# Performance work log

Hardware: AMD Instinct MI355X
Metric: run time of the kernel (lower is better)

Reference implementation:

```python
import jax, jax.numpy as jnp
import numpy as np

B, S, D = 2, 2048, 1024
H = 16
HD = D // H  # 64
THETA = 10000.0


def apply_rope(x, positions, theta):
    # x: (b, h, s, hd); positions: (s,)
    hd = x.shape[-1]
    inv_freq = theta ** (-jnp.arange(0, hd, 2, dtype=jnp.float32) / hd)  # (hd/2,)
    angles = positions.astype(jnp.float32)[:, None] * inv_freq[None, :]  # (s, hd/2)
    cos, sin = jnp.cos(angles), jnp.sin(angles)
    x1 = x[..., 0::2]
    x2 = x[..., 1::2]
    r1 = x1 * cos - x2 * sin
    r2 = x1 * sin + x2 * cos
    out = jnp.stack([r1, r2], axis=-1).reshape(x.shape)
    return out.astype(x.dtype)


def setup_inputs() -> dict:
    key = jax.random.key(0)
    ks = jax.random.split(key, 5)
    scale = 1.0 / np.sqrt(D)
    return {
        "in_features": jax.random.normal(ks[0], (B, S, D), dtype=jnp.float32),
        "token_positions": jnp.arange(S, dtype=jnp.int32),
        "Wq": jax.random.normal(ks[1], (D, D), dtype=jnp.float32) * scale,
        "Wk": jax.random.normal(ks[2], (D, D), dtype=jnp.float32) * scale,
        "Wv": jax.random.normal(ks[3], (D, D), dtype=jnp.float32) * scale,
        "Wo": jax.random.normal(ks[4], (D, D), dtype=jnp.float32) * scale,
    }


def reference(in_features, token_positions, Wq, Wk, Wv, Wo):
    b, s, d = in_features.shape
    h, hd = H, HD
    # bias-free linear: y = x @ W.T  (W is (out, in))
    q = in_features @ Wq.T
    k = in_features @ Wk.T
    v = in_features @ Wv.T
    # (b, s, h*hd) -> (b, h, s, hd)
    split = lambda t: t.reshape(b, s, h, hd).transpose(0, 2, 1, 3)
    q, k, v = split(q), split(k), split(v)
    q = apply_rope(q, token_positions, THETA)
    k = apply_rope(k, token_positions, THETA)
    scores = jnp.einsum("bhid,bhjd->bhij", q, k) / jnp.sqrt(jnp.asarray(hd, dtype=q.dtype))
    causal = jnp.triu(jnp.ones((s, s), dtype=bool), k=1)
    scores = jnp.where(causal, -jnp.inf, scores)
    attn = jax.nn.softmax(scores, axis=-1)
    out = jnp.einsum("bhij,bhjd->bhid", attn, v)
    out = out.transpose(0, 2, 1, 3).reshape(b, s, d)
    return out @ Wo.T
```

## Files before the change

### kernel.cpp

```cpp
#include <hip/hip_runtime.h>
#include <math.h>

#define NUM_HEADS 16
#define HEAD_DIM 64

typedef __bf16 bf16x8 __attribute__((ext_vector_type(8)));
typedef short shortx4 __attribute__((ext_vector_type(4)));
typedef float floatx4 __attribute__((ext_vector_type(4)));

#if __has_builtin(__builtin_amdgcn_exp2f)
#define EXP2(x) __builtin_amdgcn_exp2f(x)
#else
#define EXP2(x) exp2f(x)
#endif

__device__ __forceinline__ unsigned short f2b(float f) {
  unsigned int u = __float_as_uint(f);
  u += 0x7fffu + ((u >> 16) & 1u);
  return (unsigned short)(u >> 16);
}

__device__ __forceinline__ void async16(const void* g, void* l) {
  __builtin_amdgcn_global_load_lds(
      (const __attribute__((address_space(1))) unsigned int*)g,
      (__attribute__((address_space(3))) unsigned int*)l, 16, 0, 0);
}

__device__ __forceinline__ void cvt4(const float* in, unsigned short* out, int i) {
  float4 v = ((const float4*)in)[i];
  ushort4 o;
  o.x = f2b(v.x); o.y = f2b(v.y); o.z = f2b(v.z); o.w = f2b(v.w);
  ((ushort4*)out)[i] = o;
}

__global__ void prep(const float* __restrict__ x,
                     const float* __restrict__ w0, const float* __restrict__ w1,
                     const float* __restrict__ w2, const float* __restrict__ w3,
                     const int* __restrict__ pos,
                     unsigned short* Xb, unsigned short* o0, unsigned short* o1,
                     unsigned short* o2, unsigned short* o3,
                     float* __restrict__ tab, int xq, int w4, int ntab) {
  int i = blockIdx.x * 256 + threadIdx.x;
  int z = blockIdx.y;
  if (z == 0) {
    if (i < xq) {
#pragma unroll
      for (int rep = 0; rep < 4; ++rep) cvt4(x, Xb, rep * xq + i);
    }
  } else if (z <= 4) {
    if (i < w4) {
      const float* in = (z == 1) ? w0 : (z == 2) ? w1 : (z == 3) ? w2 : w3;
      unsigned short* out = (z == 1) ? o0 : (z == 2) ? o1 : (z == 3) ? o2 : o3;
      cvt4(in, out, i);
    }
  } else {
    if (i < ntab) {
      int fi = i & 31, s = i >> 5;
      float inv = expf(-0.28782313662425575f * (float)fi);
      float ang = (float)pos[s] * inv;
      float sn, cs;
      sincosf(ang, &sn, &cs);
      tab[i * 2] = cs;
      tab[i * 2 + 1] = sn;
    }
  }
}

template <int MODE, int MT>
__global__ __launch_bounds__(256, MODE == 1 ? 4 : 2)
void gemm_bt(const unsigned short* __restrict__ A,
             const unsigned short* __restrict__ B0,
             const unsigned short* __restrict__ B1,
             const unsigned short* __restrict__ B2,
             void* out0v, void* out1v, void* out2v,
             const float* __restrict__ ctab,
             int M, int N, int K, int S) {
  constexpr int ABUF = (MT / 16) * 512;
  constexpr int BBUF = 8 * 512;
  __shared__ unsigned short As[3 * ABUF];
  __shared__ unsigned short Bs[3 * BBUF];
  const int tid = threadIdx.x;
  const int lane = tid & 63;
  const int w = tid >> 6;
  const int lane16 = lane & 15;
  const int g = lane >> 4;
  const int wm = w >> 1, wn = w & 1;
  const int m0 = blockIdx.y * MT;
  const int n0 = blockIdx.x * 128;
  const unsigned short* Bp = (blockIdx.z == 0) ? B0 : (blockIdx.z == 1 ? B1 : B2);
  constexpr int MTILES = MT / 32;

  const floatx4 vzero = {0.f, 0.f, 0.f, 0.f};
  floatx4 acc[MTILES][4];
#pragma unroll
  for (int i = 0; i < MTILES; i++)
#pragma unroll
    for (int j = 0; j < 4; j++) acc[i][j] = vzero;

  const int ar = lane >> 2;
  const int ac = (lane & 3) * 8;

  auto stageg = [&](int k0, int sbi) {
    if constexpr (MT == 128) {
#pragma unroll
      for (int c = 0; c < 2; c++) {
        int chunk = w * 2 + c;
        async16(A  + (size_t)(m0 + chunk * 16 + ar) * K + k0 + ac, As + sbi * ABUF + chunk * 512);
        async16(Bp + (size_t)(n0 + chunk * 16 + ar) * K + k0 + ac, Bs + sbi * BBUF + chunk * 512);
      }
    } else {
      async16(A  + (size_t)(m0 + w * 16 + ar) * K + k0 + ac, As + sbi * ABUF + w * 512);
      async16(Bp + (size_t)(n0 + w * 16 + ar) * K + k0 + ac, Bs + sbi * BBUF + w * 512);
      async16(Bp + (size_t)(n0 + (w + 4) * 16 + ar) * K + k0 + ac, Bs + sbi * BBUF + (w + 4) * 512);
    }
  };

  const int NK = K >> 5;
  stageg(0, 0);
  __builtin_amdgcn_sched_barrier(0);
  if (NK > 1) stageg(32, 1);
  __builtin_amdgcn_sched_barrier(0);

  int bi = 0, si = 2;
  for (int ks = 0; ks < NK; ++ks) {
    if (ks < NK - 1) {
      if constexpr (MT == 128) asm volatile("s_waitcnt vmcnt(4)" ::: "memory");
      else                     asm volatile("s_waitcnt vmcnt(3)" ::: "memory");
    } else {
      asm volatile("s_waitcnt vmcnt(0)" ::: "memory");
    }
    __builtin_amdgcn_sched_barrier(0);
    __builtin_amdgcn_s_barrier();
    __builtin_amdgcn_sched_barrier(0);
    if (ks + 2 < NK) stageg((ks + 2) << 5, si);
    __builtin_amdgcn_sched_barrier(0);

    const unsigned short* Ab = As + bi * ABUF;
    const unsigned short* Bb = Bs + bi * BBUF;
    bf16x8 a[MTILES], b[4];
#pragma unroll
    for (int mt = 0; mt < MTILES; mt++)
      a[mt] = *(const bf16x8*)&Ab[(wm * (MT / 2) + mt * 16 + lane16) * 32 + g * 8];
#pragma unroll
    for (int nt = 0; nt < 4; nt++)
      b[nt] = *(const bf16x8*)&Bb[(wn * 64 + nt * 16 + lane16) * 32 + g * 8];
#pragma unroll
    for (int mt = 0; mt < MTILES; mt++)
#pragma unroll
      for (int nt = 0; nt < 4; nt++)
        acc[mt][nt] = __builtin_amdgcn_mfma_f32_16x16x32_bf16(b[nt], a[mt], acc[mt][nt], 0, 0, 0);

    bi = (bi == 2) ? 0 : bi + 1;
    si = (si == 2) ? 0 : si + 1;
  }

  if (MODE == 0) {
    if (blockIdx.z < 2) {
      unsigned short* outp = (unsigned short*)((blockIdx.z == 0) ? out0v : out1v);
      const float qs = (blockIdx.z == 0) ? 0.18033688011112042f : 1.0f;
#pragma unroll
      for (int mt = 0; mt < MTILES; mt++) {
        int m = m0 + wm * (MT / 2) + mt * 16 + lane16;
        int bb = m / S, s = m - bb * S;
        const float* crow = ctab + (size_t)s * 64;
#pragma unroll
        for (int nt = 0; nt < 4; nt++) {
          int n = n0 + wn * 64 + nt * 16 + g * 4;
          int h = n >> 6, dl = n & 63;
          floatx4 v = acc[mt][nt];
          float4 cs = *(const float4*)&crow[dl];
          float r0 = (v[0] * cs.x - v[1] * cs.y) * qs;
          float r1 = (v[0] * cs.y + v[1] * cs.x) * qs;
          float r2 = (v[2] * cs.z - v[3] * cs.w) * qs;
          float r3 = (v[2] * cs.w + v[3] * cs.z) * qs;
          shortx4 st;
          st[0] = (short)f2b(r0); st[1] = (short)f2b(r1);
          st[2] = (short)f2b(r2); st[3] = (short)f2b(r3);
          *(shortx4*)&outp[(((size_t)(bb * NUM_HEADS + h) * S + s) << 6) + dl] = st;
        }
      }
    } else {
      unsigned short* outp = (unsigned short*)out2v;
#pragma unroll
      for (int mt = 0; mt < MTILES; mt++) {
        int m = m0 + wm * (MT / 2) + mt * 16 + lane16;
        int bb = m / S, s = m - bb * S;
#pragma unroll
        for (int nt = 0; nt < 4; nt++) {
          int n = n0 + wn * 64 + nt * 16 + g * 4;
          int bh = bb * NUM_HEADS + (n >> 6);
          int dl = n & 63;
          size_t dbase = ((size_t)bh * 64 + dl) * S + s;
#pragma unroll
          for (int r = 0; r < 4; r++)
            outp[dbase + (size_t)r * S] = f2b(acc[mt][nt][r]);
        }
      }
    }
  } else {
    float* outp = (float*)out0v;
#pragma unroll
    for (int mt = 0; mt < MTILES; mt++) {
      int m = m0 + wm * (MT / 2) + mt * 16 + lane16;
#pragma unroll
      for (int nt = 0; nt < 4; nt++) {
        int n = n0 + wn * 64 + nt * 16 + g * 4;
        *(floatx4*)&outp[(size_t)m * N + n] = acc[mt][nt];
      }
    }
  }
}

__global__ __launch_bounds__(256, 2)
void flash_attn7(const unsigned short* __restrict__ Q,
                 const unsigned short* __restrict__ Kv,
                 const unsigned short* __restrict__ Vt,
                 unsigned short* __restrict__ Oattn, int S) {
  __shared__ unsigned short Ks[4 * 4096];
  __shared__ unsigned short Vs[4 * 4096];
  const int tid = threadIdx.x;
  const int lane = tid & 63;
  const int w = tid >> 6;
  const int lane16 = lane & 15;
  const int g = lane >> 4;
  const int sw = lane16 & 7;
  const int NT = S >> 6;
  int qa, bh;
  {
    int nx = gridDim.x, ny = gridDim.y;
    int flat = blockIdx.y * nx + blockIdx.x;
    if ((ny & 7) == 0) {
      int xcd = flat & 7;
      int idx = flat >> 3;
      int per = ny >> 3;
      bh = xcd * per + (idx % per);
      qa = idx / per;
    } else {
      qa = blockIdx.x; bh = blockIdx.y;
    }
  }
  const int qb = NT - 1 - qa;
  const int b = bh >> 4, h = bh & 15;
  const size_t kbase = (size_t)bh * S * HEAD_DIM;
  const unsigned short* Kbase = Kv + kbase;
  const unsigned short* Vtbase = Vt + (size_t)bh * HEAD_DIM * S;
  const int qrowA = qa * 64 + w * 16;
  const int qrowB = qb * 64 + w * 16;

  bf16x8 qA0, qA1, qB0, qB1;
  {
    const unsigned short* qp = Q + kbase + (size_t)(qrowA + lane16) * HEAD_DIM + g * 8;
    qA0 = *(const bf16x8*)qp;
    qA1 = *(const bf16x8*)(qp + 32);
    qp = Q + kbase + (size_t)(qrowB + lane16) * HEAD_DIM + g * 8;
    qB0 = *(const bf16x8*)qp;
    qB1 = *(const bf16x8*)(qp + 32);
  }

  const int ci0 = w * 64 + lane;
  const int ci1 = ci0 + 256;
  const int r0 = ci0 >> 3, j0 = (ci0 & 7) ^ (r0 & 7);
  const int r1 = ci1 >> 3, j1 = (ci1 & 7) ^ (r1 & 7);
  const unsigned short* kS0 = Kbase + r0 * HEAD_DIM + j0 * 8;
  const unsigned short* kS1 = Kbase + r1 * HEAD_DIM + j1 * 8;
  const unsigned short* vS0 = Vtbase + (size_t)r0 * S + j0 * 8;
  const unsigned short* vS1 = Vtbase + (size_t)r1 * S + j1 * 8;
  unsigned short* kD0 = Ks + ci0 * 8;
  unsigned short* kD1 = Ks + ci1 * 8;
  unsigned short* vD0 = Vs + ci0 * 8;
  unsigned short* vD1 = Vs + ci1 * 8;

  auto stage = [&](int t, int bi) {
    int koff = t * 4096;
    int voff = t * 64;
    int doff = bi * 4096;
    async16(kS0 + koff, kD0 + doff);
    async16(kS1 + koff, kD1 + doff);
    async16(vS0 + voff, vD0 + doff);
    async16(vS1 + voff, vD1 + doff);
  };

  const floatx4 vzero = {0.f, 0.f, 0.f, 0.f};
  floatx4 oA[4], oB[4];
#pragma unroll
  for (int i = 0; i < 4; i++) { oA[i] = vzero; oB[i] = vzero; }
  float lA = 0.f, lB = 0.f;

  stage(0, 0);
  __builtin_amdgcn_sched_barrier(0);
  if (qb >= 1) stage(1, 1);
  __builtin_amdgcn_sched_barrier(0);
  if (qb >= 2) stage(2, 2);
  __builtin_amdgcn_sched_barrier(0);

  for (int t = 0; t <= qb; ++t) {
    const int bi = t & 3;
    const int rem = qb - t;
    if (rem >= 2)      asm volatile("s_waitcnt vmcnt(8)" ::: "memory");
    else if (rem == 1) asm volatile("s_waitcnt vmcnt(4)" ::: "memory");
    else               asm volatile("s_waitcnt vmcnt(0)" ::: "memory");
    __builtin_amdgcn_sched_barrier(0);
    __builtin_amdgcn_s_barrier();
    __builtin_amdgcn_sched_barrier(0);
    if (t + 3 <= qb) stage(t + 3, (t + 3) & 3);
    __builtin_amdgcn_sched_barrier(0);

    const unsigned short* Kb_ = Ks + bi * 4096;
    const unsigned short* Vb_ = Vs + bi * 4096;
    const bool doA = (t <= qa);

    bf16x8 kf0[4], kf1[4];
#pragma unroll
    for (int c = 0; c < 4; ++c) {
      int rr = c * 16 + lane16;
      kf0[c] = *(const bf16x8*)&Kb_[(rr * 8 + (g ^ sw)) * 8];
      kf1[c] = *(const bf16x8*)&Kb_[(rr * 8 + ((4 + g) ^ sw)) * 8];
    }

    floatx4 scB[4];
#pragma unroll
    for (int c = 0; c < 4; ++c) {
      floatx4 s = vzero;
      s = __builtin_amdgcn_mfma_f32_16x16x32_bf16(kf0[c], qB0, s, 0, 0, 0);
      s = __builtin_amdgcn_mfma_f32_16x16x32_bf16(kf1[c], qB1, s, 0, 0, 0);
      scB[c] = s;
    }
    if (t == qb) {
      const int i = qrowB + lane16;
      const int jb = t * 64;
#pragma unroll
      for (int c = 0; c < 4; ++c)
#pragma unroll
        for (int r = 0; r < 4; ++r)
          if (jb + c * 16 + g * 4 + r > i) scB[c][r] = -INFINITY;
    }
    shortx4 pcB[4], pcA[4];
#pragma unroll
    for (int c = 0; c < 4; ++c) {
      float p0 = EXP2(scB[c][0]);
      float p1 = EXP2(scB[c][1]);
      float p2 = EXP2(scB[c][2]);
      float p3 = EXP2(scB[c][3]);
      lB += (p0 + p1) + (p2 + p3);
      union { unsigned int u[2]; shortx4 s4; } pu;
      pu.u[0] = __builtin_amdgcn_perm(__float_as_uint(p1), __float_as_uint(p0), 0x07060302u);
      pu.u[1] = __builtin_amdgcn_perm(__float_as_uint(p3), __float_as_uint(p2), 0x07060302u);
      pcB[c] = pu.s4;
    }

    if (doA) {
      floatx4 scA[4];
#pragma unroll
      for (int c = 0; c < 4; ++c) {
        floatx4 s = vzero;
        s = __builtin_amdgcn_mfma_f32_16x16x32_bf16(kf0[c], qA0, s, 0, 0, 0);
        s = __builtin_amdgcn_mfma_f32_16x16x32_bf16(kf1[c], qA1, s, 0, 0, 0);
        scA[c] = s;
      }
      if (t == qa) {
        const int i = qrowA + lane16;
        const int jb = t * 64;
#pragma unroll
        for (int c = 0; c < 4; ++c)
#pragma unroll
          for (int r = 0; r < 4; ++r)
            if (jb + c * 16 + g * 4 + r > i) scA[c][r] = -INFINITY;
      }
#pragma unroll
      for (int c = 0; c < 4; ++c) {
        float p0 = EXP2(scA[c][0]);
        float p1 = EXP2(scA[c][1]);
        float p2 = EXP2(scA[c][2]);
        float p3 = EXP2(scA[c][3]);
        lA += (p0 + p1) + (p2 + p3);
        union { unsigned int u[2]; shortx4 s4; } pu;
        pu.u[0] = __builtin_amdgcn_perm(__float_as_uint(p1), __float_as_uint(p0), 0x07060302u);
        pu.u[1] = __builtin_amdgcn_perm(__float_as_uint(p3), __float_as_uint(p2), 0x07060302u);
        pcA[c] = pu.s4;
      }
#pragma unroll
      for (int nt = 0; nt < 4; ++nt) {
        int rv = nt * 16 + lane16;
#pragma unroll
        for (int c = 0; c < 4; ++c) {
          shortx4 vf = *(const shortx4*)&Vb_[(rv * 8 + ((c * 2 + (g >> 1)) ^ sw)) * 8 + (g & 1) * 4];
          oB[nt] = __builtin_amdgcn_mfma_f32_16x16x16bf16_1k(vf, pcB[c], oB[nt], 0, 0, 0);
          oA[nt] = __builtin_amdgcn_mfma_f32_16x16x16bf16_1k(vf, pcA[c], oA[nt], 0, 0, 0);
        }
      }
    } else {
#pragma unroll
      for (int nt = 0; nt < 4; ++nt) {
        int rv = nt * 16 + lane16;
#pragma unroll
        for (int c = 0; c < 4; ++c) {
          shortx4 vf = *(const shortx4*)&Vb_[(rv * 8 + ((c * 2 + (g >> 1)) ^ sw)) * 8 + (g & 1) * 4];
          oB[nt] = __builtin_amdgcn_mfma_f32_16x16x16bf16_1k(vf, pcB[c], oB[nt], 0, 0, 0);
        }
      }
    }
  }

  {
    float l = lA;
    l += __shfl_xor(l, 16, 64);
    l += __shfl_xor(l, 32, 64);
    float inv = 1.0f / l;
    int srow = qrowA + lane16;
    size_t rowb = ((size_t)b * S + srow) * 1024 + h * 64;
#pragma unroll
    for (int nt = 0; nt < 4; ++nt) {
      shortx4 st;
#pragma unroll
      for (int r = 0; r < 4; ++r) st[r] = (short)f2b(oA[nt][r] * inv);
      *(shortx4*)&Oattn[rowb + nt * 16 + g * 4] = st;
    }
  }
  {
    float l = lB;
    l += __shfl_xor(l, 16, 64);
    l += __shfl_xor(l, 32, 64);
    float inv = 1.0f / l;
    int srow = qrowB + lane16;
    size_t rowb = ((size_t)b * S + srow) * 1024 + h * 64;
#pragma unroll
    for (int nt = 0; nt < 4; ++nt) {
      shortx4 st;
#pragma unroll
      for (int r = 0; r < 4; ++r) st[r] = (short)f2b(oB[nt][r] * inv);
      *(shortx4*)&Oattn[rowb + nt * 16 + g * 4] = st;
    }
  }
}

extern "C" void kernel_launch(void* const* d_in, const int* in_sizes, int n_in,
                              void* d_out, int out_size, void* d_ws, size_t ws_size,
                              hipStream_t stream) {
  const float* x  = (const float*)d_in[0];
  const int*  pos = (const int*)d_in[1];
  const float* wq = (const float*)d_in[2];
  const float* wk = (const float*)d_in[3];
  const float* wv = (const float*)d_in[4];
  const float* wo = (const float*)d_in[5];

  const int D = 1024;
  const int S = in_sizes[1];
  const int M = in_sizes[0] / D;
  const int B = M / S;
  const int BH = B * NUM_HEADS;

  char* wsb = (char*)d_ws;
  size_t off = 0;
  auto alloc = [&](size_t bytes) {
    char* p = wsb + off;
    off += (bytes + 255) & ~(size_t)255;
    return p;
  };
  unsigned short* Xb   = (unsigned short*)alloc((size_t)M * D * 2);
  unsigned short* Wqb  = (unsigned short*)alloc((size_t)D * D * 2);
  unsigned short* Wkb  = (unsigned short*)alloc((size_t)D * D * 2);
  unsigned short* Wvb  = (unsigned short*)alloc((size_t)D * D * 2);
  unsigned short* Wob  = (unsigned short*)alloc((size_t)D * D * 2);
  unsigned short* Qb   = (unsigned short*)alloc((size_t)M * D * 2);
  unsigned short* Kb   = (unsigned short*)alloc((size_t)M * D * 2);
  unsigned short* Vtb  = (unsigned short*)alloc((size_t)M * D * 2);
  unsigned short* Attn = (unsigned short*)alloc((size_t)M * D * 2);
  float*          Ctab = (float*)alloc((size_t)S * 32 * 2 * 4);
  (void)ws_size;

  {
    int n4x = M * D / 4;
    int xq = n4x / 4;
    int w4 = D * D / 4;
    int ntab = S * 32;
    int gx = (w4 + 255) / 256;
    prep<<<dim3(gx, 6), 256, 0, stream>>>(x, wq, wk, wv, wo, pos,
                                          Xb, Wqb, Wkb, Wvb, Wob, Ctab,
                                          xq, w4, ntab);
  }
  gemm_bt<0, 128><<<dim3(D / 128, M / 128, 3), 256, 0, stream>>>(
      Xb, Wqb, Wkb, Wvb, Qb, Kb, Vtb, Ctab, M, D, D, S);
  flash_attn7<<<dim3(S / 128, BH), 256, 0, stream>>>(Qb, Kb, Vtb, Attn, S);
  gemm_bt<1, 64><<<dim3(D / 128, M / 64, 1), 256, 0, stream>>>(
      Attn, Wob, Wob, Wob, d_out, d_out, d_out, Ctab, M, D, D, S);
}
```

Baseline: 180.4 us.

## Use 256-row 8-wave QKV GEMM and triple-buffer attention for occupancy

Replaces the templated QKV projection with a dedicated 512-thread kernel computing 256x128 tiles, giving each block more reuse of the B tile and halving the number of blocks. Separately, the flash attention kernel moves from four K/V LDS stages to three with rotating indices, cutting shared memory so the launch bound can rise to three blocks per CU. The cost is a shallower prefetch depth in attention and fewer, larger QKV blocks, which could leave CUs idle at the tail.

```diff
diff --git a/kernel.cpp b/kernel.cpp
--- a/kernel.cpp
+++ b/kernel.cpp
@@ -66,15 +66,131 @@
   }
 }
 
+__global__ __launch_bounds__(512, 4)
+void gemm_qkv(const unsigned short* __restrict__ A,
+              const unsigned short* __restrict__ B0,
+              const unsigned short* __restrict__ B1,
+              const unsigned short* __restrict__ B2,
+              unsigned short* __restrict__ outQ,
+              unsigned short* __restrict__ outK,
+              unsigned short* __restrict__ outV,
+              const float* __restrict__ ctab,
+              int M, int N, int K, int S) {
+  constexpr int ABUF = 16 * 512;
+  constexpr int BBUF = 8 * 512;
+  __shared__ unsigned short As[3 * ABUF];
+  __shared__ unsigned short Bs[3 * BBUF];
+  const int tid = threadIdx.x;
+  const int lane = tid & 63;
+  const int w = tid >> 6;
+  const int lane16 = lane & 15;
+  const int g = lane >> 4;
+  const int wm = w >> 1;
+  const int wn = w & 1;
+  const int m0 = blockIdx.y * 256;
+  const int n0 = blockIdx.x * 128;
+  const unsigned short* Bp = (blockIdx.z == 0) ? B0 : (blockIdx.z == 1 ? B1 : B2);
+
+  const floatx4 vzero = {0.f, 0.f, 0.f, 0.f};
+  floatx4 acc[4][4];
+#pragma unroll
+  for (int i = 0; i < 4; i++)
+#pragma unroll
+    for (int j = 0; j < 4; j++) acc[i][j] = vzero;
+
+  const int ar = lane >> 2;
+  const int ac = (lane & 3) * 8;
+
+  auto stageg = [&](int k0, int sbi) {
+    async16(A  + (size_t)(m0 + w * 16 + ar) * K + k0 + ac,        As + sbi * ABUF + w * 512);
+    async16(A  + (size_t)(m0 + (w + 8) * 16 + ar) * K + k0 + ac,  As + sbi * ABUF + (w + 8) * 512);
+    async16(Bp + (size_t)(n0 + w * 16 + ar) * K + k0 + ac,        Bs + sbi * BBUF + w * 512);
+  };
+
+  const int NK = K >> 5;
+  stageg(0, 0);
+  __builtin_amdgcn_sched_barrier(0);
+  stageg(32, 1);
+  __builtin_amdgcn_sched_barrier(0);
+
+  int bi = 0, si = 2;
+  for (int ks = 0; ks < NK; ++ks) {
+    if (ks < NK - 1) asm volatile("s_waitcnt vmcnt(3)" ::: "memory");
+    else             asm volatile("s_waitcnt vmcnt(0)" ::: "memory");
+    __builtin_amdgcn_sched_barrier(0);
+    __builtin_amdgcn_s_barrier();
+    __builtin_amdgcn_sched_barrier(0);
+    if (ks + 2 < NK) stageg((ks + 2) << 5, si);
+    __builtin_amdgcn_sched_barrier(0);
+
+    const unsigned short* Ab = As + bi * ABUF;
+    const unsigned short* Bb = Bs + bi * BBUF;
+    bf16x8 a[4], b[4];
+#pragma unroll
+    for (int mt = 0; mt < 4; mt++)
+      a[mt] = *(const bf16x8*)&Ab[(wm * 64 + mt * 16 + lane16) * 32 + g * 8];
+#pragma unroll
+    for (int nt = 0; nt < 4; nt++)
+      b[nt] = *(const bf16x8*)&Bb[(wn * 64 + nt * 16 + lane16) * 32 + g * 8];
+#pragma unroll
+    for (int mt = 0; mt < 4; mt++)
+#pragma unroll
+      for (int nt = 0; nt < 4; nt++)
+        acc[mt][nt] = __builtin_amdgcn_mfma_f32_16x16x32_bf16(b[nt], a[mt], acc[mt][nt], 0, 0, 0);
+
+    bi = (bi == 2) ? 0 : bi + 1;
+    si = (si == 2) ? 0 : si + 1;
+  }
+
+  if (blockIdx.z < 2) {
+    unsigned short* outp = (blockIdx.z == 0) ? outQ : outK;
+    const float qs = (blockIdx.z == 0) ? 0.18033688011112042f : 1.0f;
+#pragma unroll
+    for (int mt = 0; mt < 4; mt++) {
+      int m = m0 + wm * 64 + mt * 16 + lane16;
+      int bb = m / S, s = m - bb * S;
+      const float* crow = ctab + (size_t)s * 64;
+#pragma unroll
+      for (int nt = 0; nt < 4; nt++) {
+        int n = n0 + wn * 64 + nt * 16 + g * 4;
+        int h = n >> 6, dl = n & 63;
+        floatx4 v = acc[mt][nt];
+        float4 cs = *(const float4*)&crow[dl];
+        float r0 = (v[0] * cs.x - v[1] * cs.y) * qs;
+        float r1 = (v[0] * cs.y + v[1] * cs.x) * qs;
+        float r2 = (v[2] * cs.z - v[3] * cs.w) * qs;
+        float r3 = (v[2] * cs.w + v[3] * cs.z) * qs;
+        shortx4 st;
+        st[0] = (short)f2b(r0); st[1] = (short)f2b(r1);
+        st[2] = (short)f2b(r2); st[3] = (short)f2b(r3);
+        *(shortx4*)&outp[(((size_t)(bb * NUM_HEADS + h) * S + s) << 6) + dl] = st;
+      }
+    }
+  } else {
+    unsigned short* outp = outV;
+#pragma unroll
+    for (int mt = 0; mt < 4; mt++) {
+      int m = m0 + wm * 64 + mt * 16 + lane16;
+      int bb = m / S, s = m - bb * S;
+#pragma unroll
+      for (int nt = 0; nt < 4; nt++) {
+        int n = n0 + wn * 64 + nt * 16 + g * 4;
+        int bh = bb * NUM_HEADS + (n >> 6);
+        int dl = n & 63;
+        size_t dbase = ((size_t)bh * 64 + dl) * S + s;
+#pragma unroll
+        for (int r = 0; r < 4; r++)
+          outp[dbase + (size_t)r * S] = f2b(acc[mt][nt][r]);
+      }
+    }
+  }
+}
+
 template <int MODE, int MT>
 __global__ __launch_bounds__(256, MODE == 1 ? 4 : 2)
 void gemm_bt(const unsigned short* __restrict__ A,
              const unsigned short* __restrict__ B0,
-             const unsigned short* __restrict__ B1,
-             const unsigned short* __restrict__ B2,
-             void* out0v, void* out1v, void* out2v,
-             const float* __restrict__ ctab,
-             int M, int N, int K, int S) {
+             void* out0v, int M, int N, int K) {
   constexpr int ABUF = (MT / 16) * 512;
   constexpr int BBUF = 8 * 512;
   __shared__ unsigned short As[3 * ABUF];
@@ -87,7 +203,7 @@
   const int wm = w >> 1, wn = w & 1;
   const int m0 = blockIdx.y * MT;
   const int n0 = blockIdx.x * 128;
-  const unsigned short* Bp = (blockIdx.z == 0) ? B0 : (blockIdx.z == 1 ? B1 : B2);
+  const unsigned short* Bp = B0;
   constexpr int MTILES = MT / 32;
 
   const floatx4 vzero = {0.f, 0.f, 0.f, 0.f};
@@ -101,18 +217,9 @@
   const int ac = (lane & 3) * 8;
 
   auto stageg = [&](int k0, int sbi) {
-    if constexpr (MT == 128) {
-#pragma unroll
-      for (int c = 0; c < 2; c++) {
-        int chunk = w * 2 + c;
-        async16(A  + (size_t)(m0 + chunk * 16 + ar) * K + k0 + ac, As + sbi * ABUF + chunk * 512);
-        async16(Bp + (size_t)(n0 + chunk * 16 + ar) * K + k0 + ac, Bs + sbi * BBUF + chunk * 512);
-      }
-    } else {
-      async16(A  + (size_t)(m0 + w * 16 + ar) * K + k0 + ac, As + sbi * ABUF + w * 512);
-      async16(Bp + (size_t)(n0 + w * 16 + ar) * K + k0 + ac, Bs + sbi * BBUF + w * 512);
-      async16(Bp + (size_t)(n0 + (w + 4) * 16 + ar) * K + k0 + ac, Bs + sbi * BBUF + (w + 4) * 512);
-    }
+    async16(A  + (size_t)(m0 + w * 16 + ar) * K + k0 + ac, As + sbi * ABUF + w * 512);
+    async16(Bp + (size_t)(n0 + w * 16 + ar) * K + k0 + ac, Bs + sbi * BBUF + w * 512);
+    async16(Bp + (size_t)(n0 + (w + 4) * 16 + ar) * K + k0 + ac, Bs + sbi * BBUF + (w + 4) * 512);
   };
 
   const int NK = K >> 5;
@@ -123,12 +230,8 @@
 
   int bi = 0, si = 2;
   for (int ks = 0; ks < NK; ++ks) {
-    if (ks < NK - 1) {
-      if constexpr (MT == 128) asm volatile("s_waitcnt vmcnt(4)" ::: "memory");
-      else                     asm volatile("s_waitcnt vmcnt(3)" ::: "memory");
-    } else {
-      asm volatile("s_waitcnt vmcnt(0)" ::: "memory");
-    }
+    if (ks < NK - 1) asm volatile("s_waitcnt vmcnt(3)" ::: "memory");
+    else             asm volatile("s_waitcnt vmcnt(0)" ::: "memory");
     __builtin_amdgcn_sched_barrier(0);
     __builtin_amdgcn_s_barrier();
     __builtin_amdgcn_sched_barrier(0);
@@ -154,70 +257,25 @@
     si = (si == 2) ? 0 : si + 1;
   }
 
-  if (MODE == 0) {
-    if (blockIdx.z < 2) {
-      unsigned short* outp = (unsigned short*)((blockIdx.z == 0) ? out0v : out1v);
-      const float qs = (blockIdx.z == 0) ? 0.18033688011112042f : 1.0f;
-#pragma unroll
-      for (int mt = 0; mt < MTILES; mt++) {
-        int m = m0 + wm * (MT / 2) + mt * 16 + lane16;
-        int bb = m / S, s = m - bb * S;
-        const float* crow = ctab + (size_t)s * 64;
-#pragma unroll
-        for (int nt = 0; nt < 4; nt++) {
-          int n = n0 + wn * 64 + nt * 16 + g * 4;
-          int h = n >> 6, dl = n & 63;
-          floatx4 v = acc[mt][nt];
-          float4 cs = *(const float4*)&crow[dl];
-          float r0 = (v[0] * cs.x - v[1] * cs.y) * qs;
-          float r1 = (v[0] * cs.y + v[1] * cs.x) * qs;
-          float r2 = (v[2] * cs.z - v[3] * cs.w) * qs;
-          float r3 = (v[2] * cs.w + v[3] * cs.z) * qs;
-          shortx4 st;
-          st[0] = (short)f2b(r0); st[1] = (short)f2b(r1);
-          st[2] = (short)f2b(r2); st[3] = (short)f2b(r3);
-          *(shortx4*)&outp[(((size_t)(bb * NUM_HEADS + h) * S + s) << 6) + dl] = st;
-        }
-      }
-    } else {
-      unsigned short* outp = (unsigned short*)out2v;
-#pragma unroll
-      for (int mt = 0; mt < MTILES; mt++) {
-        int m = m0 + wm * (MT / 2) + mt * 16 + lane16;
-        int bb = m / S, s = m - bb * S;
-#pragma unroll
-        for (int nt = 0; nt < 4; nt++) {
-          int n = n0 + wn * 64 + nt * 16 + g * 4;
-          int bh = bb * NUM_HEADS + (n >> 6);
-          int dl = n & 63;
-          size_t dbase = ((size_t)bh * 64 + dl) * S + s;
-#pragma unroll
-          for (int r = 0; r < 4; r++)
-            outp[dbase + (size_t)r * S] = f2b(acc[mt][nt][r]);
-        }
-      }
-    }
-  } else {
-    float* outp = (float*)out0v;
-#pragma unroll
-    for (int mt = 0; mt < MTILES; mt++) {
-      int m = m0 + wm * (MT / 2) + mt * 16 + lane16;
-#pragma unroll
-      for (int nt = 0; nt < 4; nt++) {
-        int n = n0 + wn * 64 + nt * 16 + g * 4;
-        *(floatx4*)&outp[(size_t)m * N + n] = acc[mt][nt];
-      }
-    }
-  }
-}
-
-__global__ __launch_bounds__(256, 2)
+  float* outp = (float*)out0v;
+#pragma unroll
+  for (int mt = 0; mt < MTILES; mt++) {
+    int m = m0 + wm * (MT / 2) + mt * 16 + lane16;
+#pragma unroll
+    for (int nt = 0; nt < 4; nt++) {
+      int n = n0 + wn * 64 + nt * 16 + g * 4;
+      *(floatx4*)&outp[(size_t)m * N + n] = acc[mt][nt];
+    }
+  }
+}
+
+__global__ __launch_bounds__(256, 3)
 void flash_attn7(const unsigned short* __restrict__ Q,
                  const unsigned short* __restrict__ Kv,
                  const unsigned short* __restrict__ Vt,
                  unsigned short* __restrict__ Oattn, int S) {
-  __shared__ unsigned short Ks[4 * 4096];
-  __shared__ unsigned short Vs[4 * 4096];
+  __shared__ unsigned short Ks[3 * 4096];
+  __shared__ unsigned short Vs[3 * 4096];
   const int tid = threadIdx.x;
   const int lane = tid & 63;
   const int w = tid >> 6;
@@ -270,10 +328,10 @@
   unsigned short* vD0 = Vs + ci0 * 8;
   unsigned short* vD1 = Vs + ci1 * 8;
 
-  auto stage = [&](int t, int bi) {
+  auto stage = [&](int t, int sbi) {
     int koff = t * 4096;
     int voff = t * 64;
-    int doff = bi * 4096;
+    int doff = sbi * 4096;
     async16(kS0 + koff, kD0 + doff);
     async16(kS1 + koff, kD1 + doff);
     async16(vS0 + voff, vD0 + doff);
@@ -290,19 +348,16 @@
   __builtin_amdgcn_sched_barrier(0);
   if (qb >= 1) stage(1, 1);
   __builtin_amdgcn_sched_barrier(0);
-  if (qb >= 2) stage(2, 2);
-  __builtin_amdgcn_sched_barrier(0);
-
+
+  int bi = 0, si = 2;
   for (int t = 0; t <= qb; ++t) {
-    const int bi = t & 3;
     const int rem = qb - t;
-    if (rem >= 2)      asm volatile("s_waitcnt vmcnt(8)" ::: "memory");
-    else if (rem == 1) asm volatile("s_waitcnt vmcnt(4)" ::: "memory");
-    else               asm volatile("s_waitcnt vmcnt(0)" ::: "memory");
+    if (rem >= 1) asm volatile("s_waitcnt vmcnt(4)" ::: "memory");
+    else          asm volatile("s_waitcnt vmcnt(0)" ::: "memory");
     __builtin_amdgcn_sched_barrier(0);
     __builtin_amdgcn_s_barrier();
     __builtin_amdgcn_sched_barrier(0);
-    if (t + 3 <= qb) stage(t + 3, (t + 3) & 3);
+    if (t + 2 <= qb) stage(t + 2, si);
     __builtin_amdgcn_sched_barrier(0);
 
     const unsigned short* Kb_ = Ks + bi * 4096;
@@ -399,6 +454,9 @@
         }
       }
     }
+
+    bi = (bi == 2) ? 0 : bi + 1;
+    si = (si == 2) ? 0 : si + 1;
   }
 
   {
@@ -478,9 +536,9 @@
                                           Xb, Wqb, Wkb, Wvb, Wob, Ctab,
                                           xq, w4, ntab);
   }
-  gemm_bt<0, 128><<<dim3(D / 128, M / 128, 3), 256, 0, stream>>>(
+  gemm_qkv<<<dim3(D / 128, M / 256, 3), 512, 0, stream>>>(
       Xb, Wqb, Wkb, Wvb, Qb, Kb, Vtb, Ctab, M, D, D, S);
   flash_attn7<<<dim3(S / 128, BH), 256, 0, stream>>>(Qb, Kb, Vtb, Attn, S);
   gemm_bt<1, 64><<<dim3(D / 128, M / 64, 1), 256, 0, stream>>>(
-      Attn, Wob, Wob, Wob, d_out, d_out, d_out, Ctab, M, D, D, S);
-}
+      Attn, Wob, d_out, M, D, D);
+}
```

After: 209.4 us. +16.1%, slower.
